# Kernel tuning notes

Measured on AMD Instinct MI355X. Metric: run time of the kernel, lower is better.

Reference implementation:

```python
import jax, jax.numpy as jnp
import numpy as np

H = 1024          # hidden_size
NH = 16           # num_attention_heads
HD = H // NH      # head_dim = 64
CAUSAL_HEADS = 4  # causal_attention_heads
META_HEADS = NH // 4
B, S = 2, 2048
CVEC = 16
# static cognitive-state scalars (Python floats in the original dict)
CAUSAL_WEIGHT = 0.7   # > 0.5 -> causal branch active
AWARENESS = 0.9       # > 0.8 -> metacognitive branch active


def _mha(x, in_w, in_b, out_w, out_b, n_heads):
    """torch nn.MultiheadAttention (batch_first, self-attn, no mask, eval).
    in_w: [H, 3H] (pre-transposed), out_w: [H, H]."""
    b, s, h = x.shape
    hd = h // n_heads
    qkv = x @ in_w + in_b                      # [b, s, 3H]
    q, k, v = jnp.split(qkv, 3, axis=-1)
    def heads(t):
        return t.reshape(b, s, n_heads, hd).transpose(0, 2, 1, 3)  # [b, nh, s, hd]
    q, k, v = heads(q), heads(k), heads(v)
    scores = jnp.einsum('bhqd,bhkd->bhqk', q, k) / jnp.sqrt(jnp.float32(hd))
    probs = jax.nn.softmax(scores, axis=-1)
    ctx = jnp.einsum('bhqk,bhkd->bhqd', probs, v)
    ctx = ctx.transpose(0, 2, 1, 3).reshape(b, s, h)
    return ctx @ out_w + out_b


def setup_inputs() -> dict:
    key = jax.random.key(0)
    ks = jax.random.split(key, 20)
    w = lambda k, shp: (jax.random.normal(k, shp, dtype=jnp.float32) * 0.02)
    inp = {
        'hidden_states': jax.random.normal(ks[0], (B, S, H), dtype=jnp.float32),
        'attention_mask': jnp.ones((B, S), dtype=jnp.int32),
        'consciousness_vector': jax.random.uniform(ks[1], (CVEC,), dtype=jnp.float32),
        'Wq': w(ks[2], (H, H)), 'bq': jnp.zeros((H,), jnp.float32),
        'Wk': w(ks[3], (H, H)), 'bk': jnp.zeros((H,), jnp.float32),
        'Wv': w(ks[4], (H, H)), 'bv': jnp.zeros((H,), jnp.float32),
        'Wg': w(ks[5], (H, NH)), 'bg': jnp.zeros((NH,), jnp.float32),
        'Wa': w(ks[6], (CVEC, NH)), 'ba': jnp.zeros((NH,), jnp.float32),
        'ca_in_w': w(ks[7], (H, 3 * H)), 'ca_in_b': jnp.zeros((3 * H,), jnp.float32),
        'ca_out_w': w(ks[8], (H, H)), 'ca_out_b': jnp.zeros((H,), jnp.float32),
        'ma_in_w': w(ks[9], (H, 3 * H)), 'ma_in_b': jnp.zeros((3 * H,), jnp.float32),
        'ma_out_w': w(ks[10], (H, H)), 'ma_out_b': jnp.zeros((H,), jnp.float32),
        'Wo': w(ks[11], (H, H)), 'bo': jnp.zeros((H,), jnp.float32),
    }
    return inp


def reference(hidden_states, attention_mask, consciousness_vector,
              Wq, bq, Wk, bk, Wv, bv, Wg, bg, Wa, ba,
              ca_in_w, ca_in_b, ca_out_w, ca_out_b,
              ma_in_w, ma_in_b, ma_out_w, ma_out_b, Wo, bo):
    b, s, h = hidden_states.shape
    def heads(t):
        return t.reshape(b, s, NH, HD).transpose(0, 2, 1, 3)  # [b, NH, s, HD]
    q = heads(hidden_states @ Wq + bq)
    k = heads(hidden_states @ Wk + bk)
    v = heads(hidden_states @ Wv + bv)
    scores = jnp.einsum('bhqd,bhkd->bhqk', q, k) / jnp.sqrt(jnp.float32(HD))
    # consciousness modulation: sigmoid(gate(hs) + awareness(cvec)) -> [b, s, NH]
    gate = hidden_states @ Wg + bg
    awareness = consciousness_vector @ Wa + ba            # [NH]
    modulation = jax.nn.sigmoid(gate + awareness)         # [b, s, NH]
    # per-head, per-query-row scaling of scores ([b, NH, s, 1])
    scores = scores * modulation.transpose(0, 2, 1)[:, :, :, None]
    # mask: [b, s] -> [b, 1, 1, s]; masked positions -> -inf before softmax
    scores = jnp.where(attention_mask[:, None, None, :] == 0, -jnp.inf, scores)
    probs = jax.nn.softmax(scores, axis=-1)
    # dropout is identity in eval mode
    ctx = jnp.einsum('bhqk,bhkd->bhqd', probs, v)
    ctx = ctx.transpose(0, 2, 1, 3).reshape(b, s, h)
    # causal branch (causal_active > 0.5)
    causal_ctx = _mha(hidden_states, ca_in_w, ca_in_b, ca_out_w, ca_out_b, CAUSAL_HEADS)
    ctx = ctx * (1.0 - CAUSAL_WEIGHT) + causal_ctx * CAUSAL_WEIGHT
    # metacognitive branch (awareness_level > 0.8)
    meta_ctx = _mha(ctx, ma_in_w, ma_in_b, ma_out_w, ma_out_b, META_HEADS)
    mw = (AWARENESS - 0.8) / 0.2
    ctx = ctx * (1.0 - mw * 0.3) + meta_ctx * (mw * 0.3)
    return ctx @ Wo + bo
```

## Files before the change

kernel.cpp:

```cpp
#include <hip/hip_runtime.h>
#include <math.h>

#define HDIM 1024
#define NHEAD 16
#define SEQ   2048
#define BATCH 2
#define NROWS (BATCH * SEQ)
#define NEG_INF (-__builtin_inff())

typedef unsigned short u16;
typedef float  f32x4  __attribute__((ext_vector_type(4)));
typedef short  short8 __attribute__((ext_vector_type(8)));
typedef _Float16 half8 __attribute__((ext_vector_type(8)));
typedef __fp16 fp16x2 __attribute__((ext_vector_type(2)));

__device__ __forceinline__ u16 f2bf(float x) {
    unsigned u = __float_as_uint(x);
    unsigned r = u + 0x7fffu + ((u >> 16) & 1u);
    return (u16)(r >> 16);
}
__device__ __forceinline__ float bf2f(u16 h) { return __uint_as_float(((unsigned)h) << 16); }
__device__ __forceinline__ u16 f2h(float x) { _Float16 h = (_Float16)x; return *(u16*)&h; }
__device__ __forceinline__ unsigned pkh(float a, float b) {
    fp16x2 h = __builtin_amdgcn_cvt_pkrtz(a, b);
    return __builtin_bit_cast(unsigned int, h);
}
__device__ __forceinline__ float ex2(float x) { return __builtin_amdgcn_exp2f(x); }
__device__ __forceinline__ void gl_lds16(const u16* g, u16* l) {
    __builtin_amdgcn_global_load_lds((const void*)g, (void*)l, 16, 0, 0);
}

__global__ __launch_bounds__(256) void conv_f16(const float* __restrict__ src,
                                                u16* __restrict__ dst)
{
    int i8 = (blockIdx.x * 256 + threadIdx.x) * 8;
    float4 a = *(const float4*)&src[i8];
    float4 b = *(const float4*)&src[i8 + 4];
    u16 h[8] = {f2h(a.x), f2h(a.y), f2h(a.z), f2h(a.w),
                f2h(b.x), f2h(b.y), f2h(b.z), f2h(b.w)};
    uint4 p;
    p.x = h[0] | (h[1] << 16); p.y = h[2] | (h[3] << 16);
    p.z = h[4] | (h[5] << 16); p.w = h[6] | (h[7] << 16);
    *(uint4*)&dst[i8] = p;
}

__global__ __launch_bounds__(256) void mask_bias(const int* __restrict__ m,
                                                 float* __restrict__ mb)
{
    int i = blockIdx.x * 256 + threadIdx.x;
    mb[i] = m[i] ? -6.f : NEG_INF;
}

__global__ __launch_bounds__(256) void convW(const float* __restrict__ Wsrc, int ldw, int n0,
                                             int dst, u16* __restrict__ WTH, u16* __restrict__ WTL)
{
    __shared__ float tile[64][65];
    int t = threadIdx.x;
    int nb = blockIdx.x * 64, kb = blockIdx.y * 64;
    #pragma unroll
    for (int i = 0; i < 4; i++) {
        int r = (t >> 4) + i * 16, cg = t & 15;
        float4 v = *(const float4*)&Wsrc[(size_t)(kb + r) * ldw + n0 + nb + cg * 4];
        tile[r][cg * 4 + 0] = v.x; tile[r][cg * 4 + 1] = v.y;
        tile[r][cg * 4 + 2] = v.z; tile[r][cg * 4 + 3] = v.w;
    }
    __syncthreads();
    int n = t & 63, g0 = (t >> 6) * 2;
    #pragma unroll
    for (int gg = 0; gg < 2; gg++) {
        int g = g0 + gg;
        u16 hi[8], lo[8];
        #pragma unroll
        for (int u = 0; u < 8; u++) {
            float x = tile[g * 8 + u][n];
            hi[u] = f2bf(x); lo[u] = f2bf(x - bf2f(hi[u]));
        }
        size_t ob = (size_t)(dst + nb + n) * 1024 + kb + g * 8;
        uint4 ph, pl;
        ph.x = hi[0] | (hi[1] << 16); ph.y = hi[2] | (hi[3] << 16);
        ph.z = hi[4] | (hi[5] << 16); ph.w = hi[6] | (hi[7] << 16);
        pl.x = lo[0] | (lo[1] << 16); pl.y = lo[2] | (lo[3] << 16);
        pl.z = lo[4] | (lo[5] << 16); pl.w = lo[6] | (lo[7] << 16);
        *(uint4*)&WTH[ob] = ph;
        *(uint4*)&WTL[ob] = pl;
    }
}

__global__ __launch_bounds__(256) void convW3_f16(
    const float* __restrict__ w0, const float* __restrict__ w1, const float* __restrict__ w2,
    int ldw, int n0s, u16* __restrict__ WT)
{
    __shared__ float tile[64][65];
    int t = threadIdx.x;
    int z = blockIdx.z;
    const float* Wsrc = (z == 0) ? w0 : (z == 1) ? w1 : w2;
    int n0 = z * n0s, dst = z * 1024;
    int nb = blockIdx.x * 64, kb = blockIdx.y * 64;
    #pragma unroll
    for (int i = 0; i < 4; i++) {
        int r = (t >> 4) + i * 16, cg = t & 15;
        float4 v = *(const float4*)&Wsrc[(size_t)(kb + r) * ldw + n0 + nb + cg * 4];
        tile[r][cg * 4 + 0] = v.x; tile[r][cg * 4 + 1] = v.y;
        tile[r][cg * 4 + 2] = v.z; tile[r][cg * 4 + 3] = v.w;
    }
    __syncthreads();
    int n = t & 63, g0 = (t >> 6) * 2;
    #pragma unroll
    for (int gg = 0; gg < 2; gg++) {
        int g = g0 + gg;
        u16 h[8];
        #pragma unroll
        for (int u = 0; u < 8; u++) h[u] = f2h(tile[g * 8 + u][n]);
        size_t ob = (size_t)(dst + nb + n) * 1024 + kb + g * 8;
        uint4 p;
        p.x = h[0] | (h[1] << 16); p.y = h[2] | (h[3] << 16);
        p.z = h[4] | (h[5] << 16); p.w = h[6] | (h[7] << 16);
        *(uint4*)&WT[ob] = p;
    }
}

__global__ __launch_bounds__(256) void transpose_f16(
    const u16* __restrict__ in, u16* __restrict__ out)
{
    __shared__ u16 th[64][72];
    int t = threadIdx.x;
    int cb = blockIdx.x * 64;
    int rb = blockIdx.y * 64;
    {
        int r = t >> 2;
        #pragma unroll
        for (int i = 0; i < 2; i++) {
            int ck = (t & 3) + 4 * i;
            *(short8*)&th[r][ck * 8] = *(const short8*)&in[(size_t)(rb + r) * 3072 + 2048 + cb + ck * 8];
        }
    }
    __syncthreads();
    int c = t & 63, g0 = (t >> 6) * 2;
    #pragma unroll
    for (int gg = 0; gg < 2; gg++) {
        int g = g0 + gg;
        u16 hv[8];
        #pragma unroll
        for (int u = 0; u < 8; u++) hv[u] = th[g * 8 + u][c];
        size_t ob = (size_t)(cb + c) * NROWS + rb + g * 8;
        uint4 ph;
        ph.x = hv[0] | (hv[1] << 16); ph.y = hv[2] | (hv[3] << 16);
        ph.z = hv[4] | (hv[5] << 16); ph.w = hv[6] | (hv[7] << 16);
        *(uint4*)&out[ob] = ph;
    }
}

__global__ __launch_bounds__(256) void gate_f32(
    const float* __restrict__ hs, const float* __restrict__ Wg,
    const float* __restrict__ bg, const float* __restrict__ cvec,
    const float* __restrict__ Wa, const float* __restrict__ ba,
    float* __restrict__ mod)
{
    __shared__ float aw[16];
    int t = threadIdx.x;
    if (t < 16) {
        float s = ba[t];
        for (int i = 0; i < 16; i++) s = fmaf(cvec[i], Wa[i * 16 + t], s);
        aw[t] = s;
    }
    __syncthreads();
    int h = t & 15;
    int r = blockIdx.x * 16 + (t >> 4);
    const float* hrow = hs + (size_t)r * HDIM;
    float s = bg[h];
    for (int k = 0; k < HDIM; k++) s = fmaf(hrow[k], Wg[k * 16 + h], s);
    s += aw[h];
    mod[(size_t)r * 16 + h] = 1.f / (1.f + __expf(-s));
}

__global__ __launch_bounds__(256, 3) void gemm_f16(
    const u16* __restrict__ A, const u16* __restrict__ BT,
    const float* __restrict__ b0, const float* __restrict__ b1, const float* __restrict__ b2,
    u16* __restrict__ out, int M, int N, int K)
{
    __shared__ u16 aS[128][32], bS[128][32];
    int t = threadIdx.x;
    int l = t & 63, w = t >> 6;
    int lane15 = l & 15, quad = l >> 4;
    int wm = (w >> 1) * 64, wn = (w & 1) * 64;
    int m0 = blockIdx.y * 128, n0 = blockIdx.x * 128;
    int grow = w * 32 + (l >> 2);
    int gcol = (l & 3) * 8;
    f32x4 acc[4][4] = {};

    for (int k0 = 0; k0 < K; k0 += 32) {
        __syncthreads();
        #pragma unroll
        for (int j = 0; j < 2; j++) {
            gl_lds16(&A[(size_t)(m0 + grow + j * 16) * K + k0 + gcol],
                     &aS[w * 32 + j * 16][0]);
            gl_lds16(&BT[(size_t)(n0 + grow + j * 16) * K + k0 + gcol],
                     &bS[w * 32 + j * 16][0]);
        }
        __syncthreads();
        half8 af[4], bf[4];
        #pragma unroll
        for (int mt = 0; mt < 4; mt++)
            af[mt] = *(const half8*)&aS[wm + mt * 16 + lane15][quad * 8];
        #pragma unroll
        for (int nt = 0; nt < 4; nt++)
            bf[nt] = *(const half8*)&bS[wn + nt * 16 + lane15][quad * 8];
        #pragma unroll
        for (int mt = 0; mt < 4; mt++)
            #pragma unroll
            for (int nt = 0; nt < 4; nt++)
                acc[mt][nt] = __builtin_amdgcn_mfma_f32_16x16x32_f16(af[mt], bf[nt], acc[mt][nt], 0, 0, 0);
    }
    #pragma unroll
    for (int nt = 0; nt < 4; nt++) {
        int col = n0 + wn + nt * 16 + lane15;
        const float* bsel = (col < 1024) ? b0 : (col < 2048) ? b1 : b2;
        float bv = bsel[col & 1023];
        #pragma unroll
        for (int mt = 0; mt < 4; mt++)
            #pragma unroll
            for (int reg = 0; reg < 4; reg++) {
                int row = m0 + wm + mt * 16 + quad * 4 + reg;
                out[(size_t)row * N + col] = f2h(acc[mt][nt][reg] + bv);
            }
    }
}

__global__ __launch_bounds__(256, 3) void gemm_bf3(
    const u16* __restrict__ AH, const u16* __restrict__ AL,
    const u16* __restrict__ BTH, const u16* __restrict__ BTL,
    const float* __restrict__ bias,
    const u16* __restrict__ CinH, const u16* __restrict__ CinL,
    float* __restrict__ outF, u16* __restrict__ outH, u16* __restrict__ outL,
    u16* __restrict__ outX,
    int M, int N, int K, float alpha, float beta, int omode)
{
    __shared__ u16 aH[128][32], aL[128][32], bH[128][32], bL[128][32];
    int t = threadIdx.x;
    int l = t & 63, w = t >> 6;
    int lane15 = l & 15, quad = l >> 4;
    int wm = (w >> 1) * 64, wn = (w & 1) * 64;
    int m0 = blockIdx.y * 128, n0 = blockIdx.x * 128;
    int grow = w * 32 + (l >> 2);
    int gcol = (l & 3) * 8;
    f32x4 acc[4][4] = {};

    for (int k0 = 0; k0 < K; k0 += 32) {
        __syncthreads();
        #pragma unroll
        for (int j = 0; j < 2; j++) {
            size_t ga = (size_t)(m0 + grow + j * 16) * K + k0 + gcol;
            size_t gb = (size_t)(n0 + grow + j * 16) * K + k0 + gcol;
            int lr = w * 32 + j * 16;
            gl_lds16(&AH[ga],  &aH[lr][0]);
            gl_lds16(&AL[ga],  &aL[lr][0]);
            gl_lds16(&BTH[gb], &bH[lr][0]);
            gl_lds16(&BTL[gb], &bL[lr][0]);
        }
        __syncthreads();
        short8 afh[4], afl[4], bfh[4], bfl[4];
        #pragma unroll
        for (int mt = 0; mt < 4; mt++) {
            int r = wm + mt * 16 + lane15;
            afh[mt] = *(const short8*)&aH[r][quad * 8];
            afl[mt] = *(const short8*)&aL[r][quad * 8];
        }
        #pragma unroll
        for (int nt = 0; nt < 4; nt++) {
            int r = wn + nt * 16 + lane15;
            bfh[nt] = *(const short8*)&bH[r][quad * 8];
            bfl[nt] = *(const short8*)&bL[r][quad * 8];
        }
        #pragma unroll
        for (int mt = 0; mt < 4; mt++)
            #pragma unroll
            for (int nt = 0; nt < 4; nt++) {
                acc[mt][nt] = __builtin_amdgcn_mfma_f32_16x16x32_bf16(afh[mt], bfh[nt], acc[mt][nt], 0, 0, 0);
                acc[mt][nt] = __builtin_amdgcn_mfma_f32_16x16x32_bf16(afh[mt], bfl[nt], acc[mt][nt], 0, 0, 0);
                acc[mt][nt] = __builtin_amdgcn_mfma_f32_16x16x32_bf16(afl[mt], bfh[nt], acc[mt][nt], 0, 0, 0);
            }
    }
    #pragma unroll
    for (int nt = 0; nt < 4; nt++) {
        int col = n0 + wn + nt * 16 + lane15;
        float bv = bias[col];
        #pragma unroll
        for (int mt = 0; mt < 4; mt++) {
            #pragma unroll
            for (int reg = 0; reg < 4; reg++) {
                int row = m0 + wm + mt * 16 + quad * 4 + reg;
                size_t idx = (size_t)row * N + col;
                float v = alpha * (acc[mt][nt][reg] + bv);
                if (beta != 0.f) v += beta * (bf2f(CinH[idx]) + bf2f(CinL[idx]));
                if (omode == 0) outF[idx] = v;
                else {
                    u16 hb = f2bf(v);
                    outH[idx] = hb;
                    outL[idx] = f2bf(v - bf2f(hb));
                }
                if (outX) outX[idx] = f2h(v);
            }
        }
    }
}

__global__ __launch_bounds__(256, 4) void attn_main(
    const u16* __restrict__ QKV, const u16* __restrict__ VT,
    const float* __restrict__ modp, const float* __restrict__ mbias, float scale,
    u16* __restrict__ outH, u16* __restrict__ outL)
{
    constexpr int NT = SEQ / 64;
    constexpr int LD = 3 * HDIM;
    __shared__ __align__(16) u16 kb[2][64][64];
    __shared__ __align__(16) u16 vb[2][64][64];
    __shared__ __align__(16) u16 st[4][16][64];

    int t = threadIdx.x, l = t & 63, w = t >> 6;
    int lane15 = l & 15, quad = l >> 4;
    int qt0 = blockIdx.x * 64, h = blockIdx.y, b = blockIdx.z;
    int bS_ = b * SEQ;
    int sr = t >> 2, ck0 = (t & 3) * 2;
    int swz = (lane15 & 7) << 3;

    half8 qf[2];
    {
        size_t qoff = (size_t)(bS_ + qt0 + w * 16 + lane15) * LD + h * 64 + quad * 8;
        qf[0] = *(const half8*)&QKV[qoff];
        qf[1] = *(const half8*)&QKV[qoff + 32];
    }
    float smod2 = scale * 1.44269504f *
                  modp[(size_t)(bS_ + qt0 + w * 16 + lane15) * NHEAD + h];
    float lst = 0.f;
    f32x4 o[4] = {};

    short8 phK[2], phV[2];
    auto loadKV = [&](int kt) {
        size_t baseK = (size_t)(bS_ + kt + sr) * LD + HDIM + h * 64;
        phK[0] = *(const short8*)&QKV[baseK + ck0 * 8];
        phK[1] = *(const short8*)&QKV[baseK + (ck0 + 1) * 8];
        size_t baseV = (size_t)(h * 64 + sr) * NROWS + bS_ + kt;
        phV[0] = *(const short8*)&VT[baseV + ck0 * 8];
        phV[1] = *(const short8*)&VT[baseV + (ck0 + 1) * 8];
    };
    auto stage = [&](int pb_) {
        #pragma unroll
        for (int i = 0; i < 2; i++) {
            int cw = (ck0 + i) ^ (sr & 7);
            *(short8*)&kb[pb_][sr][cw * 8] = phK[i];
            *(short8*)&vb[pb_][sr][cw * 8] = phV[i];
        }
    };

    loadKV(0);

    for (int it = 0; it < NT; it++) {
        int kt = it * 64, pb = it & 1;
        stage(pb);
        __syncthreads();
        if (it + 1 < NT) loadKV(kt + 64);
        f32x4 sacc[4] = {};
        #pragma unroll
        for (int ks = 0; ks < 2; ks++)
            #pragma unroll
            for (int nb = 0; nb < 4; nb++) {
                int r = nb * 16 + lane15;
                int cw = (ks * 4 + quad) ^ (r & 7);
                half8 kf = *(const half8*)&kb[pb][r][cw * 8];
                sacc[nb] = __builtin_amdgcn_mfma_f32_16x16x32_f16(kf, qf[ks], sacc[nb], 0, 0, 0);
            }
        #pragma unroll
        for (int nb = 0; nb < 4; nb++) {
            float4 mb = *(const float4*)&mbias[bS_ + kt + nb * 16 + quad * 4];
            float p0 = ex2(fmaf(sacc[nb][0], smod2, mb.x));
            float p1 = ex2(fmaf(sacc[nb][1], smod2, mb.y));
            float p2 = ex2(fmaf(sacc[nb][2], smod2, mb.z));
            float p3 = ex2(fmaf(sacc[nb][3], smod2, mb.w));
            lst += (p0 + p1) + (p2 + p3);
            uint2 u2;
            u2.x = pkh(p0, p1);
            u2.y = pkh(p2, p3);
            *(uint2*)&st[w][lane15][(nb * 16 + quad * 4) ^ swz] = u2;
        }
        half8 pf[2];
        #pragma unroll
        for (int ks = 0; ks < 2; ks++)
            pf[ks] = *(const half8*)&st[w][lane15][(ks * 32 + quad * 8) ^ swz];
        #pragma unroll
        for (int ks = 0; ks < 2; ks++)
            #pragma unroll
            for (int nb = 0; nb < 4; nb++) {
                int r = nb * 16 + lane15;
                int cw = (ks * 4 + quad) ^ (r & 7);
                half8 vv = *(const half8*)&vb[pb][r][cw * 8];
                o[nb] = __builtin_amdgcn_mfma_f32_16x16x32_f16(pf[ks], vv, o[nb], 0, 0, 0);
            }
    }
    lst += __shfl_xor(lst, 16, 64);
    lst += __shfl_xor(lst, 32, 64);
    #pragma unroll
    for (int reg = 0; reg < 4; reg++) {
        float lv = __shfl(lst, quad * 4 + reg, 64);
        float inv = (lv > 0.f) ? 1.f / lv : 0.f;
        int row = qt0 + w * 16 + quad * 4 + reg;
        size_t rbase = (size_t)(bS_ + row) * HDIM + h * 64;
        #pragma unroll
        for (int nb = 0; nb < 4; nb++) {
            float v = o[nb][reg] * inv;
            size_t idx = rbase + nb * 16 + lane15;
            u16 hb = f2bf(v);
            outH[idx] = hb;
            outL[idx] = f2bf(v - bf2f(hb));
        }
    }
}

template <int NC>
__global__ __launch_bounds__(256, 2) void attn_f16(
    const u16* __restrict__ QKV, const u16* __restrict__ VT,
    float scale, u16* __restrict__ outH, u16* __restrict__ outL, int ldo)
{
    constexpr int HDT = NC * 64;
    constexpr int NT  = (SEQ / 2) / 64;
    constexpr int LD  = 3 * HDIM;
    __shared__ __align__(16) u16 kbuf[2][2][64][64];
    __shared__ __align__(16) u16 st[4][16][68];
    __shared__ float xl[2][16];

    int t = threadIdx.x, l = t & 63, w = t >> 6;
    int lane15 = l & 15, quad = l >> 4;
    int g = w & 1, s = w >> 1;
    int t128 = t & 127, srow = t128 >> 1, ckb = (t128 & 1) * 4;
    int qt0 = blockIdx.x * 32, h = blockIdx.y, b = blockIdx.z;
    int bS = b * SEQ, kbeg = s * (SEQ / 2);

    half8 qf[NC][2];
    {
        size_t qoff = (size_t)(bS + qt0 + g * 16 + lane15) * LD + h * HDT + quad * 8;
        #pragma unroll
        for (int c = 0; c < NC; c++)
            #pragma unroll
            for (int ks = 0; ks < 2; ks++)
                qf[c][ks] = *(const half8*)&QKV[qoff + c * 64 + ks * 32];
    }
    float sc2 = scale * 1.44269504f;
    float lst = 0.f;
    f32x4 o[NC][4] = {};

    short8 phv[4];
    auto loadK = [&](int c, int kt) {
        size_t base = (size_t)(bS + kt + srow) * LD + HDIM + h * HDT + c * 64;
        #pragma unroll
        for (int i = 0; i < 4; i++) phv[i] = *(const short8*)&QKV[base + (ckb + i) * 8];
    };
    auto loadV = [&](int c, int kt) {
        size_t base = (size_t)(h * HDT + c * 64 + srow) * NROWS + bS + kt;
        #pragma unroll
        for (int i = 0; i < 4; i++) phv[i] = *(const short8*)&VT[base + (ckb + i) * 8];
    };
    auto stor = [&](int pb_) {
        #pragma unroll
        for (int i = 0; i < 4; i++) {
            int ck = ckb + i, cw = ck ^ (srow & 7);
            *(short8*)&kbuf[pb_][s][srow][cw * 8] = phv[i];
        }
    };

    loadK(0, kbeg);
    stor(0);
    loadK(1, kbeg);
    int pb = 0;

    for (int it = 0; it < NT; it++) {
        int kt = kbeg + it * 64;
        f32x4 sacc[4] = {};
        #pragma unroll
        for (int c = 0; c < NC; c++) {
            __syncthreads();
            stor(pb ^ 1);
            if (c + 2 < NC) loadK(c + 2, kt);
            else if (c + 2 < 2 * NC) loadV(c + 2 - NC, kt);
            else if (it + 1 < NT) loadK(0, kt + 64);
            #pragma unroll
            for (int ks = 0; ks < 2; ks++)
                #pragma unroll
                for (int nb = 0; nb < 4; nb++) {
                    int r = nb * 16 + lane15;
                    int cw = (ks * 4 + quad) ^ (r & 7);
                    half8 kf = *(const half8*)&kbuf[pb][s][r][cw * 8];
                    sacc[nb] = __builtin_amdgcn_mfma_f32_16x16x32_f16(kf, qf[c][ks], sacc[nb], 0, 0, 0);
                }
            pb ^= 1;
        }
        #pragma unroll
        for (int nb = 0; nb < 4; nb++) {
            float p0 = ex2(fmaf(sacc[nb][0], sc2, -6.f));
            float p1 = ex2(fmaf(sacc[nb][1], sc2, -6.f));
            float p2 = ex2(fmaf(sacc[nb][2], sc2, -6.f));
            float p3 = ex2(fmaf(sacc[nb][3], sc2, -6.f));
            lst += (p0 + p1) + (p2 + p3);
            uint2 u2;
            u2.x = pkh(p0, p1);
            u2.y = pkh(p2, p3);
            *(uint2*)&st[w][lane15][nb * 16 + quad * 4] = u2;
        }
        half8 pf[2];
        #pragma unroll
        for (int ks = 0; ks < 2; ks++)
            pf[ks] = *(const half8*)&st[w][lane15][ks * 32 + quad * 8];
        #pragma unroll
        for (int c = 0; c < NC; c++) {
            __syncthreads();
            if (it < NT - 1 || c < NC - 1) stor(pb ^ 1);
            if (c + 2 < NC) loadV(c + 2, kt);
            else if (it + 1 < NT) {
                int p2 = c + 2 - NC;
                if (p2 < NC) loadK(p2, kt + 64); else loadV(p2 - NC, kt + 64);
            }
            #pragma unroll
            for (int ks = 0; ks < 2; ks++)
                #pragma unroll
                for (int nb = 0; nb < 4; nb++) {
                    int r = nb * 16 + lane15;
                    int cw = (ks * 4 + quad) ^ (r & 7);
                    half8 vv = *(const half8*)&kbuf[pb][s][r][cw * 8];
                    o[c][nb] = __builtin_amdgcn_mfma_f32_16x16x32_f16(pf[ks], vv, o[c][nb], 0, 0, 0);
                }
            pb ^= 1;
        }
    }
    lst += __shfl_xor(lst, 16, 64);
    lst += __shfl_xor(lst, 32, 64);
    float* xO = (float*)kbuf;
    __syncthreads();
    if (s == 1) {
        #pragma unroll
        for (int c = 0; c < NC; c++)
            #pragma unroll
            for (int nb = 0; nb < 4; nb++)
                #pragma unroll
                for (int reg = 0; reg < 4; reg++)
                    xO[(size_t)(g * 16 + quad * 4 + reg) * HDT + c * 64 + nb * 16 + lane15] = o[c][nb][reg];
        if (quad == 0) xl[g][lane15] = lst;
    }
    __syncthreads();
    if (s == 0) {
        #pragma unroll
        for (int reg = 0; reg < 4; reg++) {
            float lt = __shfl(lst, quad * 4 + reg, 64) + xl[g][quad * 4 + reg];
            float inv = (lt > 0.f) ? 1.f / lt : 0.f;
            int row = qt0 + g * 16 + quad * 4 + reg;
            size_t rbase = (size_t)(bS + row) * ldo + h * HDT;
            #pragma unroll
            for (int c = 0; c < NC; c++)
                #pragma unroll
                for (int nb = 0; nb < 4; nb++) {
                    float x1 = xO[(size_t)(g * 16 + quad * 4 + reg) * HDT + c * 64 + nb * 16 + lane15];
                    float v = (o[c][nb][reg] + x1) * inv;
                    size_t idx = rbase + c * 64 + nb * 16 + lane15;
                    u16 hb = f2bf(v);
                    outH[idx] = hb;
                    outL[idx] = f2bf(v - bf2f(hb));
                }
        }
    }
}

extern "C" void kernel_launch(void* const* d_in, const int* in_sizes, int n_in,
                              void* d_out, int out_size, void* d_ws, size_t ws_size,
                              hipStream_t stream)
{
    const float* hs   = (const float*)d_in[0];
    const int*   mask = (const int*)d_in[1];
    const float* cvec = (const float*)d_in[2];
    const float* Wq = (const float*)d_in[3];  const float* bq = (const float*)d_in[4];
    const float* Wk = (const float*)d_in[5];  const float* bk = (const float*)d_in[6];
    const float* Wv = (const float*)d_in[7];  const float* bv = (const float*)d_in[8];
    const float* Wg = (const float*)d_in[9];  const float* bg = (const float*)d_in[10];
    const float* Wa = (const float*)d_in[11]; const float* ba = (const float*)d_in[12];
    const float* caw = (const float*)d_in[13]; const float* cab = (const float*)d_in[14];
    const float* cow = (const float*)d_in[15]; const float* cob = (const float*)d_in[16];
    const float* maw = (const float*)d_in[17]; const float* mab = (const float*)d_in[18];
    const float* mow = (const float*)d_in[19]; const float* mob = (const float*)d_in[20];
    const float* Wo = (const float*)d_in[21]; const float* bo = (const float*)d_in[22];
    float* out = (float*)d_out;

    char* W = (char*)d_ws;
    const size_t MB = (size_t)1 << 20;
    u16*  QKV  = (u16*)(W + 0 * MB);
    u16*  VT   = (u16*)(W + 24 * MB);
    u16*  ctxH = (u16*)(W + 32 * MB);    u16* ctxL = (u16*)(W + 40 * MB);
    u16*  C2H  = (u16*)(W + 48 * MB);    u16* C2L  = (u16*)(W + 56 * MB);
    float* MOD = (float*)(W + 64 * MB);
    u16*  hsX  = (u16*)(W + 65 * MB);
    u16*  ctxX = (u16*)(W + 73 * MB);
    u16*  wtX  = (u16*)(W + 81 * MB);
    u16*  wtH  = (u16*)(W + 87 * MB);    u16* wtL = (u16*)(W + 89 * MB);
    float* MB_ = (float*)(W + 91 * MB);

    dim3 blk(256);
    dim3 gw(16, 16);
    dim3 gw3(16, 16, 3);
    dim3 gt(16, 64);
    dim3 gg3(24, 32);
    dim3 gg1(8, 32);
    dim3 gaM(SEQ / 64, NHEAD, BATCH);
    dim3 gaB(SEQ / 32, 4, BATCH);

    conv_f16<<<2048, blk, 0, stream>>>(hs, hsX);
    mask_bias<<<NROWS / 256, blk, 0, stream>>>(mask, MB_);
    gate_f32<<<NROWS / 16, blk, 0, stream>>>(hs, Wg, bg, cvec, Wa, ba, MOD);

    convW3_f16<<<gw3, blk, 0, stream>>>(Wq, Wk, Wv, 1024, 0, wtX);
    gemm_f16<<<gg3, blk, 0, stream>>>(hsX, wtX, bq, bk, bv, QKV, NROWS, 3072, 1024);
    transpose_f16<<<gt, blk, 0, stream>>>(QKV, VT);
    attn_main<<<gaM, blk, 0, stream>>>(QKV, VT, MOD, MB_, 0.125f, ctxH, ctxL);

    convW3_f16<<<gw3, blk, 0, stream>>>(caw, caw, caw, 3072, 1024, wtX);
    gemm_f16<<<gg3, blk, 0, stream>>>(hsX, wtX, cab, cab + 1024, cab + 2048, QKV, NROWS, 3072, 1024);
    transpose_f16<<<gt, blk, 0, stream>>>(QKV, VT);
    attn_f16<4><<<gaB, blk, 0, stream>>>(QKV, VT, 0.0625f, C2H, C2L, HDIM);
    convW<<<gw, blk, 0, stream>>>(cow, 1024, 0, 0, wtH, wtL);
    gemm_bf3<<<gg1, blk, 0, stream>>>(C2H, C2L, wtH, wtL, cob,
        ctxH, ctxL, nullptr, ctxH, ctxL, ctxX, NROWS, 1024, 1024, 0.7f, 0.3f, 1);

    convW3_f16<<<gw3, blk, 0, stream>>>(maw, maw, maw, 3072, 1024, wtX);
    gemm_f16<<<gg3, blk, 0, stream>>>(ctxX, wtX, mab, mab + 1024, mab + 2048, QKV, NROWS, 3072, 1024);
    transpose_f16<<<gt, blk, 0, stream>>>(QKV, VT);
    attn_f16<4><<<gaB, blk, 0, stream>>>(QKV, VT, 0.0625f, C2H, C2L, HDIM);
    convW<<<gw, blk, 0, stream>>>(mow, 1024, 0, 0, wtH, wtL);
    gemm_bf3<<<gg1, blk, 0, stream>>>(C2H, C2L, wtH, wtL, mob,
        ctxH, ctxL, nullptr, ctxH, ctxL, nullptr, NROWS, 1024, 1024, 0.15f, 0.85f, 1);

    convW<<<gw, blk, 0, stream>>>(Wo, 1024, 0, 0, wtH, wtL);
    gemm_bf3<<<gg1, blk, 0, stream>>>(ctxH, ctxL, wtH, wtL, bo,
        nullptr, nullptr, out, nullptr, nullptr, nullptr, NROWS, 1024, 1024, 1.f, 0.f, 0);
}
```

Measured before the change: 696.2 us.

## Double-buffer LDS tiles in f16 and split-bf16 GEMM kernels

Both GEMM kernels now keep two LDS buffers per operand. The global-to-LDS load for the next K-slice is issued before the MFMA work on the current slice, and each iteration ends with a single barrier instead of two. The aim is to hide global load latency behind matrix math and to cut barrier count. In exchange, LDS use per block doubles, so the split-bf16 kernel's launch bound drops from 3 to 2 blocks per CU, which lowers occupancy.

Result: no change. 695.5 us (-0.1%).

```diff
diff --git a/kernel.cpp b/kernel.cpp
--- a/kernel.cpp
+++ b/kernel.cpp
@@ -178,7 +178,7 @@
     const float* __restrict__ b0, const float* __restrict__ b1, const float* __restrict__ b2,
     u16* __restrict__ out, int M, int N, int K)
 {
-    __shared__ u16 aS[128][32], bS[128][32];
+    __shared__ u16 aS[2][128][32], bS[2][128][32];
     int t = threadIdx.x;
     int l = t & 63, w = t >> 6;
     int lane15 = l & 15, quad = l >> 4;
@@ -188,28 +188,35 @@
     int gcol = (l & 3) * 8;
     f32x4 acc[4][4] = {};
 
-    for (int k0 = 0; k0 < K; k0 += 32) {
-        __syncthreads();
+    auto stage = [&](int buf, int k0) {
         #pragma unroll
         for (int j = 0; j < 2; j++) {
             gl_lds16(&A[(size_t)(m0 + grow + j * 16) * K + k0 + gcol],
-                     &aS[w * 32 + j * 16][0]);
+                     &aS[buf][w * 32 + j * 16][0]);
             gl_lds16(&BT[(size_t)(n0 + grow + j * 16) * K + k0 + gcol],
-                     &bS[w * 32 + j * 16][0]);
-        }
-        __syncthreads();
+                     &bS[buf][w * 32 + j * 16][0]);
+        }
+    };
+
+    stage(0, 0);
+    __syncthreads();
+    int cur = 0;
+    for (int k0 = 0; k0 < K; k0 += 32) {
+        if (k0 + 32 < K) stage(cur ^ 1, k0 + 32);
         half8 af[4], bf[4];
         #pragma unroll
         for (int mt = 0; mt < 4; mt++)
-            af[mt] = *(const half8*)&aS[wm + mt * 16 + lane15][quad * 8];
+            af[mt] = *(const half8*)&aS[cur][wm + mt * 16 + lane15][quad * 8];
         #pragma unroll
         for (int nt = 0; nt < 4; nt++)
-            bf[nt] = *(const half8*)&bS[wn + nt * 16 + lane15][quad * 8];
+            bf[nt] = *(const half8*)&bS[cur][wn + nt * 16 + lane15][quad * 8];
         #pragma unroll
         for (int mt = 0; mt < 4; mt++)
             #pragma unroll
             for (int nt = 0; nt < 4; nt++)
                 acc[mt][nt] = __builtin_amdgcn_mfma_f32_16x16x32_f16(af[mt], bf[nt], acc[mt][nt], 0, 0, 0);
+        __syncthreads();
+        cur ^= 1;
     }
     #pragma unroll
     for (int nt = 0; nt < 4; nt++) {
@@ -226,7 +233,7 @@
     }
 }
 
-__global__ __launch_bounds__(256, 3) void gemm_bf3(
+__global__ __launch_bounds__(256, 2) void gemm_bf3(
     const u16* __restrict__ AH, const u16* __restrict__ AL,
     const u16* __restrict__ BTH, const u16* __restrict__ BTL,
     const float* __restrict__ bias,
@@ -235,7 +242,7 @@
     u16* __restrict__ outX,
     int M, int N, int K, float alpha, float beta, int omode)
 {
-    __shared__ u16 aH[128][32], aL[128][32], bH[128][32], bL[128][32];
+    __shared__ u16 aH[2][128][32], aL[2][128][32], bH[2][128][32], bL[2][128][32];
     int t = threadIdx.x;
     int l = t & 63, w = t >> 6;
     int lane15 = l & 15, quad = l >> 4;
@@ -245,31 +252,36 @@
     int gcol = (l & 3) * 8;
     f32x4 acc[4][4] = {};
 
-    for (int k0 = 0; k0 < K; k0 += 32) {
-        __syncthreads();
+    auto stage = [&](int buf, int k0) {
         #pragma unroll
         for (int j = 0; j < 2; j++) {
             size_t ga = (size_t)(m0 + grow + j * 16) * K + k0 + gcol;
             size_t gb = (size_t)(n0 + grow + j * 16) * K + k0 + gcol;
             int lr = w * 32 + j * 16;
-            gl_lds16(&AH[ga],  &aH[lr][0]);
-            gl_lds16(&AL[ga],  &aL[lr][0]);
-            gl_lds16(&BTH[gb], &bH[lr][0]);
-            gl_lds16(&BTL[gb], &bL[lr][0]);
-        }
-        __syncthreads();
+            gl_lds16(&AH[ga],  &aH[buf][lr][0]);
+            gl_lds16(&AL[ga],  &aL[buf][lr][0]);
+            gl_lds16(&BTH[gb], &bH[buf][lr][0]);
+            gl_lds16(&BTL[gb], &bL[buf][lr][0]);
+        }
+    };
+
+    stage(0, 0);
+    __syncthreads();
+    int cur = 0;
+    for (int k0 = 0; k0 < K; k0 += 32) {
+        if (k0 + 32 < K) stage(cur ^ 1, k0 + 32);
         short8 afh[4], afl[4], bfh[4], bfl[4];
         #pragma unroll
         for (int mt = 0; mt < 4; mt++) {
             int r = wm + mt * 16 + lane15;
-            afh[mt] = *(const short8*)&aH[r][quad * 8];
-            afl[mt] = *(const short8*)&aL[r][quad * 8];
+            afh[mt] = *(const short8*)&aH[cur][r][quad * 8];
+            afl[mt] = *(const short8*)&aL[cur][r][quad * 8];
         }
         #pragma unroll
         for (int nt = 0; nt < 4; nt++) {
             int r = wn + nt * 16 + lane15;
-            bfh[nt] = *(const short8*)&bH[r][quad * 8];
-            bfl[nt] = *(const short8*)&bL[r][quad * 8];
+            bfh[nt] = *(const short8*)&bH[cur][r][quad * 8];
+            bfl[nt] = *(const short8*)&bL[cur][r][quad * 8];
         }
         #pragma unroll
         for (int mt = 0; mt < 4; mt++)
@@ -279,6 +291,8 @@
                 acc[mt][nt] = __builtin_amdgcn_mfma_f32_16x16x32_bf16(afh[mt], bfl[nt], acc[mt][nt], 0, 0, 0);
                 acc[mt][nt] = __builtin_amdgcn_mfma_f32_16x16x32_bf16(afl[mt], bfh[nt], acc[mt][nt], 0, 0, 0);
             }
+        __syncthreads();
+        cur ^= 1;
     }
     #pragma unroll
     for (int nt = 0; nt < 4; nt++) {
```
